# Optimization experiments

Measured on AMD Instinct MI355X. Metric: run time of the kernel, lower is better.

Reference implementation:

```python
import jax, jax.numpy as jnp
import numpy as np

N, C, V, T = 256, 256, 25, 20
K = 3            # kernel_size
PAD = 1          # padding
O = 256          # out_channels
C4 = C // 4
EPS = 1e-5


def _bn(x, p, axes_shape):
    # p: (4, dim) = gamma, beta, running_mean, running_var (eval-mode BN)
    g, b, m, v = (p[i].reshape(axes_shape) for i in range(4))
    return (x - m) * (g / jnp.sqrt(v + EPS)) + b


def setup_inputs() -> dict:
    key = jax.random.key(0)
    ks = jax.random.split(key, 12)
    rn = lambda k, s, sc=0.05: jax.random.normal(k, s, jnp.float32) * sc
    bn = lambda k, d: jnp.stack([
        1.0 + 0.1 * jax.random.normal(jax.random.fold_in(k, 0), (d,), jnp.float32),  # gamma
        0.1 * jax.random.normal(jax.random.fold_in(k, 1), (d,), jnp.float32),        # beta
        0.1 * jax.random.normal(jax.random.fold_in(k, 2), (d,), jnp.float32),        # mean
        0.5 + jax.random.uniform(jax.random.fold_in(k, 3), (d,), jnp.float32),       # var
    ])
    return {
        "x": jax.random.normal(ks[0], (N, C, V, T), jnp.float32),
        "Wg1": rn(ks[1], (2 * T, T), 0.2),      # Linear T -> 2T (no bias)
        "Wg2": rn(ks[2], (K, 2 * T), 0.2),      # Linear 2T -> K (no bias)
        "Wl1": rn(ks[3], (C4, C, K)),           # Conv1d C -> C/4, kernel K
        "Wl2": rn(ks[4], (C, C4)),              # Conv1d C/4 -> C, kernel 1
        "Wc2": rn(ks[5], (O, C)),               # 1x1 Conv2d C -> O (no bias)
        "bng": bn(ks[6], 2 * T),
        "bnl": bn(ks[7], C4),
        "bn1p": bn(ks[8], C),
        "bn2p": bn(ks[9], O),
    }


def reference(x, Wg1, Wg2, Wl1, Wl2, Wc2, bng, bnl, bn1p, bn2p):
    n, c, v, t = x.shape
    new_x = jnp.transpose(x, (0, 1, 3, 2))            # (N, C, T, V)
    pooled = new_x.mean(axis=-1)                       # (N, C, T)  adaptive_avg_pool over V

    # --- G branch: per-(n,c) dynamic temporal kernel ---
    h = pooled.reshape(n * c, t) @ Wg1.T               # (NC, 2T)
    h = jax.nn.relu(_bn(h, bng, (1, 2 * t)))
    kern = jax.nn.softmax(h @ Wg2.T, axis=-1)          # (NC, K)
    kern = kern.reshape(n, c, K)

    # --- L branch: local temporal excitation ---
    l = jax.lax.conv_general_dilated(
        pooled, Wl1, window_strides=(1,), padding=[(K // 2, K // 2)],
        dimension_numbers=("NCH", "OIH", "NCH"))      # (N, C4, T)
    l = jax.nn.relu(_bn(l, bnl, (1, C4, 1)))
    l = jax.nn.sigmoid(jnp.einsum("oc,nct->not", Wl2, l))  # (N, C, T)
    new_x = new_x + l[..., None]                       # (N, C, T, V)

    # --- dynamic depthwise temporal conv (groups = N*C) ---
    padded = jnp.pad(new_x, ((0, 0), (0, 0), (PAD, PAD), (0, 0)))
    out = sum(kern[:, :, k, None, None] * padded[:, :, k:k + t, :] for k in range(K))

    out = jnp.transpose(out, (0, 1, 3, 2))             # (N, C, V, T)
    out = jax.nn.relu(_bn(out, bn1p, (1, c, 1, 1)))    # bn1 + relu; dropout in eval = identity
    out = jnp.einsum("oc,ncvt->novt", Wc2, out)        # 1x1 conv
    out = jax.nn.relu(_bn(out, bn2p, (1, O, 1, 1)))    # bn2 + relu
    return out
```

## Files before the change

kernel.cpp:

```cpp
#include <hip/hip_runtime.h>
#include <hip/hip_bf16.h>
#include <math.h>

#define N_ 256
#define C_ 256
#define V_ 25
#define T_ 20
#define C4_ 64
#define O_ 256
#define VT_ 500
#define EPS_ 1e-5f

typedef unsigned short ushort_t;
typedef unsigned short us4 __attribute__((ext_vector_type(4)));
typedef short short8 __attribute__((ext_vector_type(8)));
typedef float f32x4 __attribute__((ext_vector_type(4)));

__device__ __forceinline__ ushort_t f2bf(float f) {
    unsigned int u = __builtin_bit_cast(unsigned int, f);
    unsigned int r = u + 0x7fffu + ((u >> 16) & 1u);
    return (ushort_t)(r >> 16);
}

__global__ __launch_bounds__(256) void k_prep(const float* __restrict__ Wc2,
                                              ushort_t* __restrict__ wbf) {
    int i = blockIdx.x * 256 + threadIdx.x;
    f32x4 v = ((const f32x4*)Wc2)[i];
    us4 o; o.x = f2bf(v.x); o.y = f2bf(v.y); o.z = f2bf(v.z); o.w = f2bf(v.w);
    ((us4*)wbf)[i] = o;
}

#define YSTRIDE 264

__global__ __launch_bounds__(256, 1) void k_mega(const float* __restrict__ x,
                                                 const ushort_t* __restrict__ wbf,
                                                 const float* __restrict__ Wg1,
                                                 const float* __restrict__ Wg2,
                                                 const float* __restrict__ Wl1,
                                                 const float* __restrict__ Wl2,
                                                 const float* __restrict__ bng,
                                                 const float* __restrict__ bnl,
                                                 const float* __restrict__ bn1p,
                                                 const float* __restrict__ bn2p,
                                                 float* __restrict__ out) {
    __shared__ __align__(16) char smem[61184];
    float (*pp)[22] = (float(*)[22])(smem);
    float* wg1 = (float*)(smem + 22528);
    float* wg2 = (float*)(smem + 25728);
    float* sg  = (float*)(smem + 26208);
    float* bg  = (float*)(smem + 26368);
    float (*ls)[20] = (float(*)[20])(smem + 26528);
    float* sl  = (float*)(smem + 31648);
    float* bl  = (float*)(smem + 31904);
    ushort_t* yT = (ushort_t*)(smem);
    float* outs  = (float*)(smem);
    float* s2t = (float*)(smem + 59136);
    float* b2t = (float*)(smem + 60160);

    int tid = threadIdx.x;
    int n = blockIdx.x;
    const float* xn = x + n * (C_ * V_ * T_);

    for (int i = tid; i < 800; i += 256) wg1[i] = Wg1[i];
    if (tid < 120) wg2[tid] = Wg2[tid];
    if (tid < 40) {
        float g = bng[tid], b = bng[40 + tid];
        float m = bng[80 + tid], v = bng[120 + tid];
        float s = g * rsqrtf(v + EPS_);
        sg[tid] = s; bg[tid] = b - m * s;
    }
    if (tid < C4_) {
        float g = bnl[tid], b = bnl[64 + tid];
        float m = bnl[128 + tid], v = bnl[192 + tid];
        float s = g * rsqrtf(v + EPS_);
        sl[tid] = s; bl[tid] = b - m * s;
    }

    {
        f32x4 pacc[5];
        const float* pbase[5];
        int pc[5], ptq[5];
#pragma unroll
        for (int k = 0; k < 5; ++k) {
            int s = tid + 256 * k;
            pc[k] = s / 5; ptq[k] = s % 5;
            pbase[k] = xn + pc[k] * (V_ * T_) + ptq[k] * 4;
            pacc[k] = (f32x4){0.f, 0.f, 0.f, 0.f};
        }
#pragma unroll 5
        for (int v = 0; v < V_; ++v) {
#pragma unroll
            for (int k = 0; k < 5; ++k)
                pacc[k] += *(const f32x4*)(pbase[k] + v * T_);
        }
#pragma unroll
        for (int k = 0; k < 5; ++k) {
            int c = pc[k], t1 = ptq[k] * 4 + 1;
            pp[c][t1 + 0] = pacc[k].x * 0.04f;
            pp[c][t1 + 1] = pacc[k].y * 0.04f;
            pp[c][t1 + 2] = pacc[k].z * 0.04f;
            pp[c][t1 + 3] = pacc[k].w * 0.04f;
        }
        pp[tid][0] = 0.f; pp[tid][21] = 0.f;
    }
    __syncthreads();

    float k0, k1, k2, s1, b1;
    {
        int c = tid;
        float p[20];
#pragma unroll
        for (int t = 0; t < 20; ++t) p[t] = pp[c][t + 1];
        float l0 = 0.f, l1 = 0.f, l2 = 0.f;
#pragma unroll 4
        for (int j = 0; j < 40; ++j) {
            float h = 0.f;
#pragma unroll
            for (int t = 0; t < 20; ++t) h = fmaf(wg1[j * 20 + t], p[t], h);
            h = fmaxf(fmaf(h, sg[j], bg[j]), 0.f);
            l0 = fmaf(wg2[j], h, l0);
            l1 = fmaf(wg2[40 + j], h, l1);
            l2 = fmaf(wg2[80 + j], h, l2);
        }
        float mx = fmaxf(l0, fmaxf(l1, l2));
        float e0 = __expf(l0 - mx), e1 = __expf(l1 - mx), e2 = __expf(l2 - mx);
        float inv = 1.f / (e0 + e1 + e2);
        k0 = e0 * inv; k1 = e1 * inv; k2 = e2 * inv;

        float g1 = bn1p[c], be1 = bn1p[256 + c];
        float m1 = bn1p[512 + c], v1 = bn1p[768 + c];
        s1 = g1 * rsqrtf(v1 + EPS_);
        b1 = be1 - m1 * s1;
        float g2 = bn2p[c], be2 = bn2p[256 + c];
        float m2 = bn2p[512 + c], v2 = bn2p[768 + c];
        float s2 = g2 * rsqrtf(v2 + EPS_);
        s2t[c] = s2; b2t[c] = be2 - m2 * s2;
    }

    {
        int c4 = tid >> 2;
        int t0 = (tid & 3) * 5;
        float acc0 = 0.f, acc1 = 0.f, acc2 = 0.f, acc3 = 0.f, acc4 = 0.f;
        const float* w = Wl1 + c4 * (C_ * 3);
#pragma unroll 8
        for (int c = 0; c < C_; ++c) {
            float w0 = w[c * 3 + 0];
            float w1 = w[c * 3 + 1];
            float w2 = w[c * 3 + 2];
            float a0 = pp[c][t0 + 0], a1 = pp[c][t0 + 1], a2 = pp[c][t0 + 2];
            float a3 = pp[c][t0 + 3], a4 = pp[c][t0 + 4], a5 = pp[c][t0 + 5];
            float a6 = pp[c][t0 + 6];
            acc0 = fmaf(w0, a0, fmaf(w1, a1, fmaf(w2, a2, acc0)));
            acc1 = fmaf(w0, a1, fmaf(w1, a2, fmaf(w2, a3, acc1)));
            acc2 = fmaf(w0, a2, fmaf(w1, a3, fmaf(w2, a4, acc2)));
            acc3 = fmaf(w0, a3, fmaf(w1, a4, fmaf(w2, a5, acc3)));
            acc4 = fmaf(w0, a4, fmaf(w1, a5, fmaf(w2, a6, acc4)));
        }
        float s = sl[c4], b = bl[c4];
        ls[c4][t0 + 0] = fmaxf(fmaf(acc0, s, b), 0.f);
        ls[c4][t0 + 1] = fmaxf(fmaf(acc1, s, b), 0.f);
        ls[c4][t0 + 2] = fmaxf(fmaf(acc2, s, b), 0.f);
        ls[c4][t0 + 3] = fmaxf(fmaf(acc3, s, b), 0.f);
        ls[c4][t0 + 4] = fmaxf(fmaf(acc4, s, b), 0.f);
    }
    __syncthreads();

    float l2r[20];
    {
        int c = tid;
#pragma unroll
        for (int t = 0; t < 20; ++t) l2r[t] = 0.f;
        const float* w = Wl2 + c * C4_;
#pragma unroll 4
        for (int c4 = 0; c4 < C4_; ++c4) {
            float wv = w[c4];
#pragma unroll
            for (int t = 0; t < 20; ++t) l2r[t] = fmaf(wv, ls[c4][t], l2r[t]);
        }
#pragma unroll
        for (int t = 0; t < 20; ++t) l2r[t] = 1.f / (1.f + __expf(-l2r[t]));
    }
    __syncthreads();

    int lane = tid & 63;
    int wave = tid >> 6;
    int mrow = lane & 15;
    int kof = (lane >> 4) * 8;
    int prow = (lane >> 4) * 4;
    int obase = wave * 64;
    float* outn = out + n * (O_ * VT_);

    for (int vblk = 0; vblk < 5; ++vblk) {
        {
            int c = tid;
            const float* xp = xn + (c * V_ + vblk * 5) * T_;
#pragma unroll
            for (int vl = 0; vl < 5; ++vl) {
                float a[22];
                a[0] = 0.f; a[21] = 0.f;
                const f32x4* xv = (const f32x4*)(xp + vl * T_);
#pragma unroll
                for (int q = 0; q < 5; ++q) {
                    f32x4 u = xv[q];
                    a[q*4 + 1] = u.x + l2r[q*4 + 0];
                    a[q*4 + 2] = u.y + l2r[q*4 + 1];
                    a[q*4 + 3] = u.z + l2r[q*4 + 2];
                    a[q*4 + 4] = u.w + l2r[q*4 + 3];
                }
                ushort_t* yrow = yT + (vl * 20) * YSTRIDE + c;
#pragma unroll
                for (int t = 0; t < 20; ++t) {
                    float z = fmaf(k0, a[t], fmaf(k1, a[t + 1], k2 * a[t + 2]));
                    float y = fmaxf(fmaf(z, s1, b1), 0.f);
                    yrow[t * YSTRIDE] = f2bf(y);
                }
            }
        }
        for (int i = tid; i < 12 * YSTRIDE; i += 256) yT[100 * YSTRIDE + i] = 0;
        __syncthreads();

        f32x4 acc[4][7];
#pragma unroll
        for (int mt = 0; mt < 4; ++mt)
#pragma unroll
            for (int ct = 0; ct < 7; ++ct) acc[mt][ct] = (f32x4){0.f, 0.f, 0.f, 0.f};

#pragma unroll 2
        for (int kk = 0; kk < C_; kk += 32) {
            short8 af[4];
            short8 bfr[7];
#pragma unroll
            for (int mt = 0; mt < 4; ++mt)
                af[mt] = *(const short8*)(wbf + (obase + mt * 16 + mrow) * C_ + kk + kof);
#pragma unroll
            for (int ct = 0; ct < 7; ++ct)
                bfr[ct] = *(const short8*)(yT + (ct * 16 + mrow) * YSTRIDE + kk + kof);
#pragma unroll
            for (int mt = 0; mt < 4; ++mt)
#pragma unroll
                for (int ct = 0; ct < 7; ++ct)
                    acc[mt][ct] = __builtin_amdgcn_mfma_f32_16x16x32_bf16(af[mt], bfr[ct], acc[mt][ct], 0, 0, 0);
        }
        __syncthreads();

#pragma unroll
        for (int P = 0; P < 2; ++P) {
#pragma unroll
            for (int mtl = 0; mtl < 2; ++mtl) {
                int mt = 2 * P + mtl;
#pragma unroll
                for (int ct = 0; ct < 7; ++ct) {
                    int pl = ct * 16 + mrow;
                    if (pl < 100) {
#pragma unroll
                        for (int r = 0; r < 4; ++r) {
                            int og = obase + mt * 16 + prow + r;
                            int oo = wave * 32 + mtl * 16 + prow + r;
                            outs[oo * 100 + pl] =
                                fmaxf(fmaf(acc[mt][ct][r], s2t[og], b2t[og]), 0.f);
                        }
                    }
                }
            }
            __syncthreads();
            for (int i = tid; i < 3200; i += 256) {
                int oo = i / 25, col = i % 25;
                int og = (oo >> 5) * 64 + P * 32 + (oo & 31);
                *(f32x4*)(outn + og * VT_ + vblk * 100 + col * 4) = ((const f32x4*)outs)[i];
            }
            __syncthreads();
        }
    }
}

extern "C" void kernel_launch(void* const* d_in, const int* in_sizes, int n_in,
                              void* d_out, int out_size, void* d_ws, size_t ws_size,
                              hipStream_t stream) {
    const float* x   = (const float*)d_in[0];
    const float* Wg1 = (const float*)d_in[1];
    const float* Wg2 = (const float*)d_in[2];
    const float* Wl1 = (const float*)d_in[3];
    const float* Wl2 = (const float*)d_in[4];
    const float* Wc2 = (const float*)d_in[5];
    const float* bng = (const float*)d_in[6];
    const float* bnl = (const float*)d_in[7];
    const float* bn1p = (const float*)d_in[8];
    const float* bn2p = (const float*)d_in[9];
    float* out = (float*)d_out;

    ushort_t* wbf = (ushort_t*)d_ws;

    k_prep<<<dim3(64), dim3(256), 0, stream>>>(Wc2, wbf);
    k_mega<<<dim3(N_), dim3(256), 0, stream>>>(x, wbf, Wg1, Wg2, Wl1, Wl2,
                                               bng, bnl, bn1p, bn2p, out);
}
```

Before: 374.2 us.

## Split fused kernel into pool, gating, and per-vblock main kernels

The single per-sample kernel is split into three. A wide pooling kernel also handles the bf16 conversion of Wc2. A per-sample kernel computes the dynamic temporal kernel and the sigmoid excitation and writes them to workspace. The main kernel is launched over (5 v-blocks × N) with two blocks per CU. The aim is to replace a 256-block grid that runs the pooling, gating and five GEMM phases serially with many more independent blocks, which should improve latency hiding and CU utilisation. In exchange it adds workspace round-trips, extra launches, and rounding of x to bf16 before the excitation is added, which costs some precision.

```diff
diff --git a/kernel.cpp b/kernel.cpp
--- a/kernel.cpp
+++ b/kernel.cpp
@@ -16,50 +16,61 @@
 typedef short short8 __attribute__((ext_vector_type(8)));
 typedef float f32x4 __attribute__((ext_vector_type(4)));
 
+__device__ __forceinline__ float bf2f(ushort_t u) {
+    unsigned int v = ((unsigned int)u) << 16;
+    return __builtin_bit_cast(float, v);
+}
 __device__ __forceinline__ ushort_t f2bf(float f) {
     unsigned int u = __builtin_bit_cast(unsigned int, f);
     unsigned int r = u + 0x7fffu + ((u >> 16) & 1u);
     return (ushort_t)(r >> 16);
 }
 
-__global__ __launch_bounds__(256) void k_prep(const float* __restrict__ Wc2,
+__global__ __launch_bounds__(256) void k_pool(const float* __restrict__ x,
+                                              float* __restrict__ pooled,
+                                              const float* __restrict__ Wc2,
                                               ushort_t* __restrict__ wbf) {
-    int i = blockIdx.x * 256 + threadIdx.x;
-    f32x4 v = ((const f32x4*)Wc2)[i];
-    us4 o; o.x = f2bf(v.x); o.y = f2bf(v.y); o.z = f2bf(v.z); o.w = f2bf(v.w);
-    ((us4*)wbf)[i] = o;
-}
-
-#define YSTRIDE 264
-
-__global__ __launch_bounds__(256, 1) void k_mega(const float* __restrict__ x,
-                                                 const ushort_t* __restrict__ wbf,
-                                                 const float* __restrict__ Wg1,
-                                                 const float* __restrict__ Wg2,
-                                                 const float* __restrict__ Wl1,
-                                                 const float* __restrict__ Wl2,
-                                                 const float* __restrict__ bng,
-                                                 const float* __restrict__ bnl,
-                                                 const float* __restrict__ bn1p,
-                                                 const float* __restrict__ bn2p,
-                                                 float* __restrict__ out) {
-    __shared__ __align__(16) char smem[61184];
-    float (*pp)[22] = (float(*)[22])(smem);
-    float* wg1 = (float*)(smem + 22528);
-    float* wg2 = (float*)(smem + 25728);
-    float* sg  = (float*)(smem + 26208);
-    float* bg  = (float*)(smem + 26368);
-    float (*ls)[20] = (float(*)[20])(smem + 26528);
-    float* sl  = (float*)(smem + 31648);
-    float* bl  = (float*)(smem + 31904);
-    ushort_t* yT = (ushort_t*)(smem);
-    float* outs  = (float*)(smem);
-    float* s2t = (float*)(smem + 59136);
-    float* b2t = (float*)(smem + 60160);
-
+    int tid = threadIdx.x;
+    if (blockIdx.x >= 8192) {
+        int i = (blockIdx.x - 8192) * 256 + tid;
+        f32x4 v = ((const f32x4*)Wc2)[i];
+        us4 o; o.x = f2bf(v.x); o.y = f2bf(v.y); o.z = f2bf(v.z); o.w = f2bf(v.w);
+        ((us4*)wbf)[i] = o;
+        return;
+    }
+    __shared__ float xs[8][504];
+    const f32x4* src = (const f32x4*)(x + (size_t)blockIdx.x * 8 * VT_);
+    for (int i = tid; i < 1000; i += 256) {
+        int r = i / 125, cidx = (i % 125) * 4;
+        *(f32x4*)&xs[r][cidx] = src[i];
+    }
+    __syncthreads();
+    if (tid < 160) {
+        int r = tid / 20, t = tid % 20;
+        float s = 0.f;
+#pragma unroll
+        for (int v = 0; v < V_; ++v) s += xs[r][v * T_ + t];
+        pooled[blockIdx.x * 160 + tid] = s * 0.04f;
+    }
+}
+
+__global__ __launch_bounds__(256) void k_gl(const float* __restrict__ pooled,
+                                            const float* __restrict__ Wg1,
+                                            const float* __restrict__ Wg2,
+                                            const float* __restrict__ Wl1,
+                                            const float* __restrict__ Wl2,
+                                            const float* __restrict__ bng,
+                                            const float* __restrict__ bnl,
+                                            float* __restrict__ kern,
+                                            float* __restrict__ l2out) {
+    __shared__ float pp[C_][22];
+    __shared__ float wg1[800];
+    __shared__ float wg2[120];
+    __shared__ float sg[40], bg[40];
+    __shared__ float ls[C4_][20];
+    __shared__ float sl[C4_], bl[C4_];
     int tid = threadIdx.x;
     int n = blockIdx.x;
-    const float* xn = x + n * (C_ * V_ * T_);
 
     for (int i = tid; i < 800; i += 256) wg1[i] = Wg1[i];
     if (tid < 120) wg2[tid] = Wg2[tid];
@@ -75,37 +86,20 @@
         float s = g * rsqrtf(v + EPS_);
         sl[tid] = s; bl[tid] = b - m * s;
     }
-
-    {
-        f32x4 pacc[5];
-        const float* pbase[5];
-        int pc[5], ptq[5];
-#pragma unroll
-        for (int k = 0; k < 5; ++k) {
-            int s = tid + 256 * k;
-            pc[k] = s / 5; ptq[k] = s % 5;
-            pbase[k] = xn + pc[k] * (V_ * T_) + ptq[k] * 4;
-            pacc[k] = (f32x4){0.f, 0.f, 0.f, 0.f};
-        }
-#pragma unroll 5
-        for (int v = 0; v < V_; ++v) {
-#pragma unroll
-            for (int k = 0; k < 5; ++k)
-                pacc[k] += *(const f32x4*)(pbase[k] + v * T_);
-        }
-#pragma unroll
-        for (int k = 0; k < 5; ++k) {
-            int c = pc[k], t1 = ptq[k] * 4 + 1;
-            pp[c][t1 + 0] = pacc[k].x * 0.04f;
-            pp[c][t1 + 1] = pacc[k].y * 0.04f;
-            pp[c][t1 + 2] = pacc[k].z * 0.04f;
-            pp[c][t1 + 3] = pacc[k].w * 0.04f;
+    {
+        const f32x4* pn = (const f32x4*)(pooled + n * (C_ * T_));
+#pragma unroll
+        for (int q = 0; q < 5; ++q) {
+            int id = q * 256 + tid;
+            int c = id / 5, qq = id % 5;
+            f32x4 v = pn[id];
+            pp[c][qq * 4 + 1] = v.x; pp[c][qq * 4 + 2] = v.y;
+            pp[c][qq * 4 + 3] = v.z; pp[c][qq * 4 + 4] = v.w;
         }
         pp[tid][0] = 0.f; pp[tid][21] = 0.f;
     }
     __syncthreads();
 
-    float k0, k1, k2, s1, b1;
     {
         int c = tid;
         float p[20];
@@ -125,16 +119,8 @@
         float mx = fmaxf(l0, fmaxf(l1, l2));
         float e0 = __expf(l0 - mx), e1 = __expf(l1 - mx), e2 = __expf(l2 - mx);
         float inv = 1.f / (e0 + e1 + e2);
-        k0 = e0 * inv; k1 = e1 * inv; k2 = e2 * inv;
-
-        float g1 = bn1p[c], be1 = bn1p[256 + c];
-        float m1 = bn1p[512 + c], v1 = bn1p[768 + c];
-        s1 = g1 * rsqrtf(v1 + EPS_);
-        b1 = be1 - m1 * s1;
-        float g2 = bn2p[c], be2 = bn2p[256 + c];
-        float m2 = bn2p[512 + c], v2 = bn2p[768 + c];
-        float s2 = g2 * rsqrtf(v2 + EPS_);
-        s2t[c] = s2; b2t[c] = be2 - m2 * s2;
+        float* kp = kern + (n * C_ + c) * 3;
+        kp[0] = e0 * inv; kp[1] = e1 * inv; kp[2] = e2 * inv;
     }
 
     {
@@ -165,21 +151,107 @@
     }
     __syncthreads();
 
-    float l2r[20];
     {
         int c = tid;
-#pragma unroll
-        for (int t = 0; t < 20; ++t) l2r[t] = 0.f;
+        float acc[20];
+#pragma unroll
+        for (int t = 0; t < 20; ++t) acc[t] = 0.f;
         const float* w = Wl2 + c * C4_;
 #pragma unroll 4
         for (int c4 = 0; c4 < C4_; ++c4) {
             float wv = w[c4];
 #pragma unroll
-            for (int t = 0; t < 20; ++t) l2r[t] = fmaf(wv, ls[c4][t], l2r[t]);
-        }
-#pragma unroll
-        for (int t = 0; t < 20; ++t) l2r[t] = 1.f / (1.f + __expf(-l2r[t]));
-    }
+            for (int t = 0; t < 20; ++t) acc[t] = fmaf(wv, ls[c4][t], acc[t]);
+        }
+        f32x4* o = (f32x4*)(l2out + (n * C_ + c) * T_);
+#pragma unroll
+        for (int q = 0; q < 5; ++q) {
+            f32x4 v;
+            v.x = 1.f / (1.f + __expf(-acc[q*4+0]));
+            v.y = 1.f / (1.f + __expf(-acc[q*4+1]));
+            v.z = 1.f / (1.f + __expf(-acc[q*4+2]));
+            v.w = 1.f / (1.f + __expf(-acc[q*4+3]));
+            o[q] = v;
+        }
+    }
+}
+
+#define YSTRIDE 264
+
+__global__ __launch_bounds__(256, 2) void k_main(const float* __restrict__ x,
+                                                 const ushort_t* __restrict__ wbf,
+                                                 const float* __restrict__ bn1p,
+                                                 const float* __restrict__ bn2p,
+                                                 const float* __restrict__ kern,
+                                                 const float* __restrict__ l2g,
+                                                 float* __restrict__ out) {
+    __shared__ __align__(16) char smem[61184];
+    ushort_t* yT  = (ushort_t*)smem;
+    float*    outs = (float*)smem;
+    float* s2t = (float*)(smem + 59136);
+    float* b2t = (float*)(smem + 60160);
+
+    int tid = threadIdx.x;
+    int n = blockIdx.y;
+    int vblk = blockIdx.x;
+    const float* xn = x + n * (C_ * V_ * T_);
+
+    float s1, b1, k0, k1, k2, l2r[20];
+    {
+        int c = tid;
+        float g1 = bn1p[c], be1 = bn1p[256 + c];
+        float m1 = bn1p[512 + c], v1 = bn1p[768 + c];
+        s1 = g1 * rsqrtf(v1 + EPS_);
+        b1 = be1 - m1 * s1;
+        float g2 = bn2p[c], be2 = bn2p[256 + c];
+        float m2 = bn2p[512 + c], v2 = bn2p[768 + c];
+        float s2 = g2 * rsqrtf(v2 + EPS_);
+        s2t[c] = s2; b2t[c] = be2 - m2 * s2;
+        const float* kp = kern + (n * C_ + c) * 3;
+        k0 = kp[0]; k1 = kp[1]; k2 = kp[2];
+        const f32x4* lp = (const f32x4*)(l2g + (n * C_ + c) * T_);
+#pragma unroll
+        for (int q = 0; q < 5; ++q) {
+            f32x4 v = lp[q];
+            l2r[q*4+0] = v.x; l2r[q*4+1] = v.y; l2r[q*4+2] = v.z; l2r[q*4+3] = v.w;
+        }
+    }
+
+    for (int vl = 0; vl < 5; ++vl) {
+        ushort_t* xs = yT + (vl * 20) * YSTRIDE;
+#pragma unroll
+        for (int q = 0; q < 5; ++q) {
+            int id = q * 256 + tid;
+            int c = id / 5, qq = id % 5;
+            f32x4 v = *(const f32x4*)(xn + c * VT_ + vblk * 100 + vl * 20 + qq * 4);
+            us4 o; o.x = f2bf(v.x); o.y = f2bf(v.y); o.z = f2bf(v.z); o.w = f2bf(v.w);
+            *(us4*)(xs + c * 20 + qq * 4) = o;
+        }
+        __syncthreads();
+        float a[22];
+        a[0] = 0.f; a[21] = 0.f;
+        {
+            const ushort_t* xrow = xs + tid * 20;
+#pragma unroll
+            for (int qq = 0; qq < 5; ++qq) {
+                us4 u = *(const us4*)(xrow + qq * 4);
+                a[qq*4 + 1] = bf2f(u.x) + l2r[qq*4 + 0];
+                a[qq*4 + 2] = bf2f(u.y) + l2r[qq*4 + 1];
+                a[qq*4 + 3] = bf2f(u.z) + l2r[qq*4 + 2];
+                a[qq*4 + 4] = bf2f(u.w) + l2r[qq*4 + 3];
+            }
+        }
+        __syncthreads();
+        {
+            ushort_t* yrow = yT + (vl * 20) * YSTRIDE + tid;
+#pragma unroll
+            for (int t = 0; t < 20; ++t) {
+                float z = fmaf(k0, a[t], fmaf(k1, a[t + 1], k2 * a[t + 2]));
+                yrow[t * YSTRIDE] = f2bf(fmaxf(fmaf(z, s1, b1), 0.f));
+            }
+        }
+    }
+    for (int i = tid; i < 12 * YSTRIDE; i += 256) yT[100 * YSTRIDE + i] = 0;
     __syncthreads();
 
     int lane = tid & 63;
@@ -188,88 +260,58 @@
     int kof = (lane >> 4) * 8;
     int prow = (lane >> 4) * 4;
     int obase = wave * 64;
+
+    f32x4 acc[4][7];
+#pragma unroll
+    for (int mt = 0; mt < 4; ++mt)
+#pragma unroll
+        for (int ct = 0; ct < 7; ++ct) acc[mt][ct] = (f32x4){0.f, 0.f, 0.f, 0.f};
+
+#pragma unroll 2
+    for (int kk = 0; kk < C_; kk += 32) {
+        short8 af[4];
+        short8 bfr[7];
+#pragma unroll
+        for (int mt = 0; mt < 4; ++mt)
+            af[mt] = *(const short8*)(wbf + (obase + mt * 16 + mrow) * C_ + kk + kof);
+#pragma unroll
+        for (int ct = 0; ct < 7; ++ct)
+            bfr[ct] = *(const short8*)(yT + (ct * 16 + mrow) * YSTRIDE + kk + kof);
+#pragma unroll
+        for (int mt = 0; mt < 4; ++mt)
+#pragma unroll
+            for (int ct = 0; ct < 7; ++ct)
+                acc[mt][ct] = __builtin_amdgcn_mfma_f32_16x16x32_bf16(af[mt], bfr[ct], acc[mt][ct], 0, 0, 0);
+    }
+    __syncthreads();
+
     float* outn = out + n * (O_ * VT_);
-
-    for (int vblk = 0; vblk < 5; ++vblk) {
-        {
-            int c = tid;
-            const float* xp = xn + (c * V_ + vblk * 5) * T_;
-#pragma unroll
-            for (int vl = 0; vl < 5; ++vl) {
-                float a[22];
-                a[0] = 0.f; a[21] = 0.f;
-                const f32x4* xv = (const f32x4*)(xp + vl * T_);
-#pragma unroll
-                for (int q = 0; q < 5; ++q) {
-                    f32x4 u = xv[q];
-                    a[q*4 + 1] = u.x + l2r[q*4 + 0];
-                    a[q*4 + 2] = u.y + l2r[q*4 + 1];
-                    a[q*4 + 3] = u.z + l2r[q*4 + 2];
-                    a[q*4 + 4] = u.w + l2r[q*4 + 3];
-                }
-                ushort_t* yrow = yT + (vl * 20) * YSTRIDE + c;
-#pragma unroll
-                for (int t = 0; t < 20; ++t) {
-                    float z = fmaf(k0, a[t], fmaf(k1, a[t + 1], k2 * a[t + 2]));
-                    float y = fmaxf(fmaf(z, s1, b1), 0.f);
-                    yrow[t * YSTRIDE] = f2bf(y);
-                }
-            }
-        }
-        for (int i = tid; i < 12 * YSTRIDE; i += 256) yT[100 * YSTRIDE + i] = 0;
-        __syncthreads();
-
-        f32x4 acc[4][7];
-#pragma unroll
-        for (int mt = 0; mt < 4; ++mt)
-#pragma unroll
-            for (int ct = 0; ct < 7; ++ct) acc[mt][ct] = (f32x4){0.f, 0.f, 0.f, 0.f};
-
-#pragma unroll 2
-        for (int kk = 0; kk < C_; kk += 32) {
-            short8 af[4];
-            short8 bfr[7];
-#pragma unroll
-            for (int mt = 0; mt < 4; ++mt)
-                af[mt] = *(const short8*)(wbf + (obase + mt * 16 + mrow) * C_ + kk + kof);
-#pragma unroll
-            for (int ct = 0; ct < 7; ++ct)
-                bfr[ct] = *(const short8*)(yT + (ct * 16 + mrow) * YSTRIDE + kk + kof);
-#pragma unroll
-            for (int mt = 0; mt < 4; ++mt)
-#pragma unroll
-                for (int ct = 0; ct < 7; ++ct)
-                    acc[mt][ct] = __builtin_amdgcn_mfma_f32_16x16x32_bf16(af[mt], bfr[ct], acc[mt][ct], 0, 0, 0);
-        }
-        __syncthreads();
-
-#pragma unroll
-        for (int P = 0; P < 2; ++P) {
-#pragma unroll
-            for (int mtl = 0; mtl < 2; ++mtl) {
-                int mt = 2 * P + mtl;
-#pragma unroll
-                for (int ct = 0; ct < 7; ++ct) {
-                    int pl = ct * 16 + mrow;
-                    if (pl < 100) {
-#pragma unroll
-                        for (int r = 0; r < 4; ++r) {
-                            int og = obase + mt * 16 + prow + r;
-                            int oo = wave * 32 + mtl * 16 + prow + r;
-                            outs[oo * 100 + pl] =
-                                fmaxf(fmaf(acc[mt][ct][r], s2t[og], b2t[og]), 0.f);
-                        }
+#pragma unroll
+    for (int P = 0; P < 2; ++P) {
+#pragma unroll
+        for (int mtl = 0; mtl < 2; ++mtl) {
+            int mt = 2 * P + mtl;
+#pragma unroll
+            for (int ct = 0; ct < 7; ++ct) {
+                int pl = ct * 16 + mrow;
+                if (pl < 100) {
+#pragma unroll
+                    for (int r = 0; r < 4; ++r) {
+                        int og = obase + mt * 16 + prow + r;
+                        int oo = wave * 32 + mtl * 16 + prow + r;
+                        outs[oo * 100 + pl] =
+                            fmaxf(fmaf(acc[mt][ct][r], s2t[og], b2t[og]), 0.f);
                     }
                 }
             }
-            __syncthreads();
-            for (int i = tid; i < 3200; i += 256) {
-                int oo = i / 25, col = i % 25;
-                int og = (oo >> 5) * 64 + P * 32 + (oo & 31);
-                *(f32x4*)(outn + og * VT_ + vblk * 100 + col * 4) = ((const f32x4*)outs)[i];
-            }
-            __syncthreads();
-        }
+        }
+        __syncthreads();
+        for (int i = tid; i < 3200; i += 256) {
+            int oo = i / 25, col = i % 25;
+            int og = (oo >> 5) * 64 + P * 32 + (oo & 31);
+            *(f32x4*)(outn + og * VT_ + vblk * 100 + col * 4) = ((const f32x4*)outs)[i];
+        }
+        __syncthreads();
     }
 }
 
@@ -288,9 +330,13 @@
     const float* bn2p = (const float*)d_in[9];
     float* out = (float*)d_out;
 
-    ushort_t* wbf = (ushort_t*)d_ws;
-
-    k_prep<<<dim3(64), dim3(256), 0, stream>>>(Wc2, wbf);
-    k_mega<<<dim3(N_), dim3(256), 0, stream>>>(x, wbf, Wg1, Wg2, Wl1, Wl2,
-                                               bng, bnl, bn1p, bn2p, out);
-}
+    float* ws = (float*)d_ws;
+    float* pooled = ws;
+    float* kern   = ws + 1310720;
+    float* l2g    = ws + 1310720 + 196608;
+    ushort_t* wbf = (ushort_t*)(ws + 1310720 + 196608 + 1310720);
+
+    k_pool<<<dim3(8256), dim3(256), 0, stream>>>(x, pooled, Wc2, wbf);
+    k_gl<<<dim3(N_), dim3(256), 0, stream>>>(pooled, Wg1, Wg2, Wl1, Wl2, bng, bnl, kern, l2g);
+    k_main<<<dim3(5, N_), dim3(256), 0, stream>>>(x, wbf, bn1p, bn2p, kern, l2g, out);
+}
```

Result: faster. 364.8 us (-2.5%).
